# Optimization experiments

Measured on AMD Instinct MI355X. Metric: run time of the kernel, lower is better.

The kernel has to match this reference:

```python
import jax, jax.numpy as jnp
import numpy as np

B, T = 64, 20          # batch, caption length
C, HW = 512, 196       # cnn_channels, width*height (14x14)
V, E, U = 10000, 256, 512  # n_tokens, emb_size, lstm_units
MAX_NORM = 5.0


def setup_inputs() -> dict:
    key = jax.random.key(0)
    ks = jax.random.split(key, 12)
    s = 0.02
    return {
        "image_features": jax.random.normal(ks[0], (B, C, HW), jnp.float32),
        "captions_ix": jax.random.randint(ks[1], (B, T), 0, V, dtype=jnp.int32),
        "W_h0": jax.random.normal(ks[2], (U, C), jnp.float32) * s,
        "b_h0": jnp.zeros((U,), jnp.float32),
        "W_c0": jax.random.normal(ks[3], (U, C), jnp.float32) * s,
        "b_c0": jnp.zeros((U,), jnp.float32),
        "emb": jax.random.normal(ks[4], (V, E), jnp.float32) * s,
        "W_key": jax.random.normal(ks[5], (U, C), jnp.float32) * s,
        "b_key": jnp.zeros((U,), jnp.float32),
        "W_ih": jax.random.normal(ks[6], (4 * U, C + E), jnp.float32) * s,
        "b_ih": jnp.zeros((4 * U,), jnp.float32),
        "W_hh": jax.random.normal(ks[7], (4 * U, U), jnp.float32) * s,
        "b_hh": jnp.zeros((4 * U,), jnp.float32),
        "W_out": jax.random.normal(ks[8], (V, C + E + U), jnp.float32) * s,
        "b_out": jnp.zeros((V,), jnp.float32),
    }


def _caption_net(image_features, captions_ix, W_h0, b_h0, W_c0, b_c0, emb,
                 W_key, b_key, W_ih, b_ih, W_hh, b_hh, W_out, b_out):
    feats_mean = image_features.mean(axis=2)                # [B, C]
    hid0 = feats_mean @ W_h0.T + b_h0                       # [B, U]
    cell0 = feats_mean @ W_c0.T + b_c0                      # [B, U]
    feats = jnp.transpose(image_features, (0, 2, 1))        # [B, HW, C]
    keys = feats @ W_key.T + b_key                          # [B, HW, U]

    # nn.Embedding(max_norm=5): renorm rows whose L2 norm exceeds 5
    norms = jnp.linalg.norm(emb, axis=1, keepdims=True)
    emb_eff = emb * jnp.minimum(1.0, MAX_NORM / jnp.maximum(norms, 1e-12))
    cap_emb = emb_eff[captions_ix]                          # [B, T, E]

    inv_scale = 1.0 / (keys.shape[2] ** 0.5)

    def step(carry, emb_t):
        hid, cell = carry
        # scaled dot-product attention, query = current hidden state
        scores = jnp.einsum('bu,bku->bk', hid, keys) * inv_scale   # [B, HW]
        w = jax.nn.softmax(scores, axis=1)
        a = jnp.einsum('bk,bkc->bc', w, feats)                     # [B, C]
        x = jnp.concatenate([emb_t, a], axis=1)                    # [B, E+C]
        gates = x @ W_ih.T + b_ih + hid @ W_hh.T + b_hh            # [B, 4U]
        i, f, g, o = jnp.split(gates, 4, axis=1)
        cell = jax.nn.sigmoid(f) * cell + jax.nn.sigmoid(i) * jnp.tanh(g)
        hid = jax.nn.sigmoid(o) * jnp.tanh(cell)
        out = jnp.concatenate([hid, a, emb_t], axis=1)             # [B, U+C+E]
        return (hid, cell), (out, w)

    (_, _), (outs, attn) = jax.lax.scan(step, (hid0, cell0),
                                        jnp.transpose(cap_emb, (1, 0, 2)))
    outs = jnp.transpose(outs, (1, 0, 2))                   # [B, T, U+C+E]
    attn = jnp.transpose(attn, (1, 0, 2))                   # [B, T, HW]
    logits = outs @ W_out.T + b_out                         # [B, T, V]
    return logits, attn


def reference(image_features, captions_ix, W_h0, b_h0, W_c0, b_c0, emb,
              W_key, b_key, W_ih, b_ih, W_hh, b_hh, W_out, b_out):
    return _caption_net(image_features, captions_ix, W_h0, b_h0, W_c0, b_c0,
                        emb, W_key, b_key, W_ih, b_ih, W_hh, b_hh, W_out, b_out)
```

## Files before the change

### kernel.cpp

```cpp
#include <hip/hip_runtime.h>
#include <math.h>

#define B 64
#define T 20
#define C 512
#define HW 196
#define V 10000
#define E 256
#define U 512
#define G4U 2048
#define ODIM 1280
#define KTOT 1280
#define NBLK 64

typedef short bf8_t __attribute__((ext_vector_type(8)));
typedef float f4_t  __attribute__((ext_vector_type(4)));

__device__ __forceinline__ unsigned short f2bf(float f) {
    unsigned int u = __float_as_uint(f);
    return (unsigned short)((u + 0x7fffu + ((u >> 16) & 1u)) >> 16);
}
__device__ __forceinline__ float bf2f(unsigned short s) {
    return __uint_as_float((unsigned int)s << 16);
}
__device__ __forceinline__ float bflo(unsigned int kv) { return __uint_as_float(kv << 16); }
__device__ __forceinline__ float bfhi(unsigned int kv) { return __uint_as_float(kv & 0xffff0000u); }

__device__ __forceinline__ void coh_load4x2(const void* p0, const void* p1,
                                            uint4& r0, uint4& r1) {
    asm volatile("global_load_dwordx4 %0, %2, off sc0 sc1\n\t"
                 "global_load_dwordx4 %1, %3, off sc0 sc1\n\t"
                 "s_waitcnt vmcnt(0)"
                 : "=&v"(r0), "=&v"(r1) : "v"(p0), "v"(p1) : "memory");
}
__device__ __forceinline__ void coh_load4_issue(const void* p, uint4& r) {
    asm volatile("global_load_dwordx4 %0, %1, off sc0 sc1"
                 : "=&v"(r) : "v"(p) : "memory");
}
__device__ __forceinline__ void wait_vm0() {
    asm volatile("s_waitcnt vmcnt(0)" ::: "memory");
    __builtin_amdgcn_sched_barrier(0);
}
__device__ __forceinline__ void coh_store1f(void* p, float v) {
    asm volatile("global_store_dword %0, %1, off sc0 sc1" :: "v"(p), "v"(v) : "memory");
}
__device__ __forceinline__ void coh_store1u(void* p, unsigned int v) {
    asm volatile("global_store_dword %0, %1, off sc0 sc1" :: "v"(p), "v"(v) : "memory");
}
__device__ __forceinline__ void coh_store_us(void* p, unsigned int v) {
    asm volatile("global_store_short %0, %1, off sc0 sc1" :: "v"(p), "v"(v) : "memory");
}

__device__ __forceinline__ void gbar(int* bar) {
    asm volatile("s_waitcnt vmcnt(0)" ::: "memory");
    __syncthreads();
    if (threadIdx.x == 0) {
        int g = __hip_atomic_load(bar + 1, __ATOMIC_RELAXED, __HIP_MEMORY_SCOPE_AGENT);
        if (__hip_atomic_fetch_add(bar, 1, __ATOMIC_RELAXED, __HIP_MEMORY_SCOPE_AGENT) == NBLK - 1) {
            __hip_atomic_store(bar, 0, __ATOMIC_RELAXED, __HIP_MEMORY_SCOPE_AGENT);
            __hip_atomic_store(bar + 1, g + 1, __ATOMIC_RELEASE, __HIP_MEMORY_SCOPE_AGENT);
        } else {
            while (__hip_atomic_load(bar + 1, __ATOMIC_RELAXED, __HIP_MEMORY_SCOPE_AGENT) == g)
                __builtin_amdgcn_s_sleep(1);
        }
    }
    __syncthreads();
}

__global__ void k_mean(const float* __restrict__ img, float* __restrict__ fm,
                       int* __restrict__ bar) {
    if (blockIdx.x == 0 && threadIdx.x == 0) { bar[0] = 0; bar[1] = 0; }
    int wave = threadIdx.x >> 6;
    int lane = threadIdx.x & 63;
    int row = blockIdx.x * 4 + wave;
    const float* p = img + (size_t)row * HW;
    float s = p[lane] + p[lane + 64] + p[lane + 128];
    if (lane < 4) s += p[lane + 192];
    for (int off = 32; off > 0; off >>= 1) s += __shfl_down(s, off, 64);
    if (lane == 0) fm[row] = s * (1.0f / HW);
}

__global__ void k_init(const float* __restrict__ fm,
                       const float* __restrict__ W_h0, const float* __restrict__ b_h0,
                       const float* __restrict__ W_c0, const float* __restrict__ b_c0,
                       unsigned short* __restrict__ xb, float* __restrict__ cell) {
    int wv = blockIdx.x * 4 + (threadIdx.x >> 6);
    int lane = threadIdx.x & 63;
    int which = wv >> 15;
    int r = wv & 32767;
    int b = r >> 9, u = r & 511;
    const float* W = which ? W_c0 : W_h0;
    const float* bias = which ? b_c0 : b_h0;
    const float* f = fm + b * C;
    const float* w = W + (size_t)u * C;
    float s = 0.f;
    #pragma unroll
    for (int c = 0; c < C; c += 64) s += f[c + lane] * w[c + lane];
    for (int off = 32; off > 0; off >>= 1) s += __shfl_down(s, off, 64);
    if (lane == 0) {
        float v = s + bias[u];
        if (which) cell[r] = v;
        else       xb[(size_t)b * KTOT + 768 + u] = f2bf(v);
    }
}

__global__ void k_wkt(const float* __restrict__ Wk, float* __restrict__ WkT) {
    __shared__ float tile[64][65];
    int u0 = blockIdx.x * 64, c0 = blockIdx.y * 64;
    int x = threadIdx.x & 63, y0 = threadIdx.x >> 6;
    #pragma unroll
    for (int i = 0; i < 16; i++) {
        int r = y0 * 16 + i;
        tile[r][x] = Wk[(size_t)(u0 + r) * C + c0 + x];
    }
    __syncthreads();
    #pragma unroll
    for (int i = 0; i < 16; i++) {
        int r = y0 * 16 + i;
        WkT[(size_t)(c0 + r) * U + u0 + x] = tile[x][r];
    }
}

__global__ __launch_bounds__(256) void k_keys(const float* __restrict__ img,
        const float* __restrict__ WkT, const float* __restrict__ b_key,
        unsigned short* __restrict__ keys2) {
    __shared__ unsigned short st[32][200];
    int b = blockIdx.x >> 4;
    int u0 = (blockIdx.x & 15) * 32;
    int wave = __builtin_amdgcn_readfirstlane(threadIdx.x >> 6);
    int lane = threadIdx.x & 63;
    int lk = lane < 49 ? lane : 48;
    const f4_t* imgb = (const f4_t*)(img + (size_t)b * C * HW);
    f4_t acc[8];
    #pragma unroll
    for (int j = 0; j < 8; j++) acc[j] = (f4_t){0.f, 0.f, 0.f, 0.f};
    const float* wp = WkT + u0 + wave * 8;
    for (int c = 0; c < C; c++) {
        f4_t v = imgb[c * 49 + lk];
        const float* w = wp + (size_t)c * U;
        #pragma unroll
        for (int j = 0; j < 8; j++) acc[j] += v * w[j];
    }
    if (lane < 49) {
        #pragma unroll
        for (int j = 0; j < 8; j++) {
            float bk = b_key[u0 + wave * 8 + j];
            int ul = wave * 8 + j;
            int k = lane * 4;
            st[ul][k + 0] = f2bf(acc[j].x + bk);
            st[ul][k + 1] = f2bf(acc[j].y + bk);
            st[ul][k + 2] = f2bf(acc[j].z + bk);
            st[ul][k + 3] = f2bf(acc[j].w + bk);
        }
    }
    __syncthreads();
    int ui = threadIdx.x & 15;
    int kr = threadIdx.x >> 4;
    #pragma unroll
    for (int pass = 0; pass < 13; pass++) {
        int k = pass * 16 + kr;
        if (k < HW) {
            unsigned int lo = st[ui * 2][k];
            unsigned int hi = st[ui * 2 + 1][k];
            *(unsigned int*)&keys2[((size_t)b * HW + k) * U + u0 + ui * 2] = (hi << 16) | lo;
        }
    }
}

__global__ void k_wg(const float* __restrict__ W_ih, const float* __restrict__ W_hh,
                     unsigned short* __restrict__ Wg) {
    int j = blockIdx.x;
    int tid = threadIdx.x;
    const float* s1 = W_ih + (size_t)j * 768;
    const float* s2 = W_hh + (size_t)j * 512;
    unsigned short* dst = Wg + (size_t)j * KTOT;
    #pragma unroll
    for (int p = 0; p < 3; p++) dst[tid + p * 256] = f2bf(s1[tid + p * 256]);
    #pragma unroll
    for (int p = 0; p < 2; p++) dst[768 + tid + p * 256] = f2bf(s2[tid + p * 256]);
}

__global__ void k_emb(const int* __restrict__ ix, const float* __restrict__ emb,
                      unsigned short* __restrict__ outs) {
    int bt = blockIdx.x;
    int e = threadIdx.x;
    int row = ix[bt];
    float v = emb[(size_t)row * E + e];
    __shared__ float red[4];
    float sq = v * v;
    for (int off = 32; off > 0; off >>= 1) sq += __shfl_down(sq, off, 64);
    int wave = e >> 6, lane = e & 63;
    if (lane == 0) red[wave] = sq;
    __syncthreads();
    float norm = sqrtf(red[0] + red[1] + red[2] + red[3]);
    float scale = fminf(1.0f, 5.0f / fmaxf(norm, 1e-12f));
    outs[(size_t)bt * ODIM + (U + C) + e] = f2bf(v * scale);
}

__global__ __launch_bounds__(256) void k_wo(const float* __restrict__ W,
                                            unsigned short* __restrict__ Wb) {
    size_t i = ((size_t)blockIdx.x * 256 + threadIdx.x) * 8;
    float4 f0 = *(const float4*)(W + i);
    float4 f1 = *(const float4*)(W + i + 4);
    uint4 q;
    q.x = ((unsigned int)f2bf(f0.y) << 16) | f2bf(f0.x);
    q.y = ((unsigned int)f2bf(f0.w) << 16) | f2bf(f0.z);
    q.z = ((unsigned int)f2bf(f1.y) << 16) | f2bf(f1.x);
    q.w = ((unsigned int)f2bf(f1.w) << 16) | f2bf(f1.z);
    *(uint4*)(Wb + i) = q;
}

__global__ __launch_bounds__(256) void k_loop(
    unsigned short* __restrict__ outs, unsigned short* __restrict__ xb,
    const float* __restrict__ cell0, float* __restrict__ gates4,
    const unsigned short* __restrict__ keys2, const float* __restrict__ img,
    const float* __restrict__ b_ih, const float* __restrict__ b_hh,
    const unsigned short* __restrict__ Wg, float* __restrict__ attn,
    int* __restrict__ bar) {
    int b = blockIdx.x;
    int tid = threadIdx.x;
    int wave = __builtin_amdgcn_readfirstlane(tid >> 6);
    int lane = tid & 63;
    int m16 = lane & 15, quad = lane >> 4;
    __shared__ float hidS[U];
    __shared__ float wS[256];
    __shared__ float red[4];
    __shared__ unsigned short As2[64][72];
    __shared__ unsigned short Bs2[32][72];

    float c_r[2], bsum[2][4];
    #pragma unroll
    for (int p = 0; p < 2; p++) {
        int u = tid + p * 256;
        c_r[p] = cell0[(size_t)b * U + u];
        #pragma unroll
        for (int q = 0; q < 4; q++)
            bsum[p][q] = b_ih[q * 512 + u] + b_hh[q * 512 + u];
    }

    int j0g = blockIdx.x * 32;
    int r = tid >> 2, kq = tid & 3;
    int rb = tid >> 3, kb = tid & 7;
    int n16 = wave & 1, mpair = wave >> 1;

    for (int t = 0; t <= T; ++t) {
        if (t > 0) {
            const float* g0 = gates4 + (size_t)b * 2048 + tid * 4;
            uint4 r0, r1;
            coh_load4x2(g0, g0 + 1024, r0, r1);
            #pragma unroll
            for (int p = 0; p < 2; p++) {
                int u = tid + p * 256;
                float4 gv = p ? *(float4*)&r1 : *(float4*)&r0;
                float g0f = gv.x + bsum[p][0];
                float g1f = gv.y + bsum[p][1];
                float g2f = gv.z + bsum[p][2];
                float g3f = gv.w + bsum[p][3];
                float si = 1.f / (1.f + expf(-g0f));
                float sf = 1.f / (1.f + expf(-g1f));
                float tg = tanhf(g2f);
                float so = 1.f / (1.f + expf(-g3f));
                float cn = sf * c_r[p] + si * tg;
                c_r[p] = cn;
                float hn = so * tanhf(cn);
                hidS[u] = hn;
                unsigned int hv = f2bf(hn);
                outs[((size_t)b * T + (t - 1)) * ODIM + u] = (unsigned short)hv;
                coh_store_us(&xb[(size_t)b * KTOT + 768 + u], hv);
            }
        } else {
            #pragma unroll
            for (int p = 0; p < 2; p++) {
                int u = tid + p * 256;
                hidS[u] = bf2f(xb[(size_t)b * KTOT + 768 + u]);
            }
        }
        if (t == T) break;
        __syncthreads();

        float sc = 0.f;
        if (tid < HW) {
            const uint4* kr = (const uint4*)(keys2 + ((size_t)b * HW + tid) * U);
            float acc = 0.f;
            #pragma unroll 8
            for (int i = 0; i < 64; i++) {
                uint4 kv = kr[i];
                float4 h0 = *(const float4*)&hidS[i * 8];
                float4 h1 = *(const float4*)&hidS[i * 8 + 4];
                acc += bflo(kv.x) * h0.x + bfhi(kv.x) * h0.y
                     + bflo(kv.y) * h0.z + bfhi(kv.y) * h0.w
                     + bflo(kv.z) * h1.x + bfhi(kv.z) * h1.y
                     + bflo(kv.w) * h1.z + bfhi(kv.w) * h1.w;
            }
            sc = acc * 0.044194173824159216f;
        }
        {
            float v = (tid < HW) ? sc : -1e30f;
            float m = v;
            for (int off = 32; off > 0; off >>= 1) m = fmaxf(m, __shfl_down(m, off, 64));
            if (lane == 0) red[wave] = m;
            __syncthreads();
            m = fmaxf(fmaxf(red[0], red[1]), fmaxf(red[2], red[3]));
            float ex = (tid < HW) ? expf(v - m) : 0.f;
            float ssum = ex;
            for (int off = 32; off > 0; off >>= 1) ssum += __shfl_down(ssum, off, 64);
            __syncthreads();
            if (lane == 0) red[wave] = ssum;
            __syncthreads();
            ssum = red[0] + red[1] + red[2] + red[3];
            float w = ex / ssum;
            wS[tid] = w;
            if (tid < HW) attn[((size_t)b * T + t) * HW + tid] = w;
        }
        __syncthreads();

        {
            const float4* imgb = (const float4*)(img + (size_t)b * C * HW);
            #pragma unroll
            for (int p = 0; p < 2; p++) {
                int c = tid + p * 256;
                const float4* rr4 = imgb + c * 49;
                float acc = 0.f;
                for (int k4 = 0; k4 < 49; k4++) {
                    float4 vv = rr4[k4];
                    acc += wS[4 * k4] * vv.x + wS[4 * k4 + 1] * vv.y
                         + wS[4 * k4 + 2] * vv.z + wS[4 * k4 + 3] * vv.w;
                }
                unsigned int av = f2bf(acc);
                coh_store_us(&xb[(size_t)b * KTOT + 256 + c], av);
                outs[((size_t)b * T + t) * ODIM + U + c] = (unsigned short)av;
            }
        }
        if (tid < 128) {
            const unsigned int* src = (const unsigned int*)(outs + ((size_t)b * T + t) * ODIM);
            unsigned int* dst = (unsigned int*)(xb + (size_t)b * KTOT);
            coh_store1u(&dst[tid], src[512 + tid]);
        }

        gbar(bar);

        {
            f4_t acc2[2];
            acc2[0] = (f4_t){0.f, 0.f, 0.f, 0.f};
            acc2[1] = (f4_t){0.f, 0.f, 0.f, 0.f};
            const unsigned short* xrow = xb + (size_t)r * KTOT + kq * 16;
            const unsigned short* wrow = Wg + (size_t)(j0g + rb) * KTOT + kb * 8;
            uint4 a0, a1, bq;
            coh_load4x2(xrow, xrow + 8, a0, a1);
            bq = *(const uint4*)wrow;
            for (int k0 = 0; k0 < KTOT; k0 += 64) {
                *(uint4*)&As2[r][kq * 16]     = a0;
                *(uint4*)&As2[r][kq * 16 + 8] = a1;
                *(uint4*)&Bs2[rb][kb * 8]     = bq;
                __syncthreads();
                uint4 na0, na1, nbq;
                bool more = (k0 + 64 < KTOT);
                if (more) {
                    coh_load4_issue(xrow + k0 + 64, na0);
                    coh_load4_issue(xrow + k0 + 64 + 8, na1);
                    nbq = *(const uint4*)(wrow + k0 + 64);
                }
                #pragma unroll
                for (int h = 0; h < 2; h++) {
                    bf8_t bfr = *(const bf8_t*)&Bs2[n16 * 16 + m16][h * 32 + quad * 8];
                    #pragma unroll
                    for (int i2 = 0; i2 < 2; i2++) {
                        bf8_t afr = *(const bf8_t*)&As2[(mpair * 2 + i2) * 16 + m16][h * 32 + quad * 8];
                        acc2[i2] = __builtin_amdgcn_mfma_f32_16x16x32_bf16(afr, bfr, acc2[i2], 0, 0, 0);
                    }
                }
                if (more) {
                    wait_vm0();
                    a0 = na0; a1 = na1; bq = nbq;
                }
                __syncthreads();
            }
            int n = j0g + n16 * 16 + m16;
            int qq = n >> 9, uu = n & 511;
            float* gbase = gates4 + (size_t)uu * 4 + qq;
            #pragma unroll
            for (int i2 = 0; i2 < 2; i2++) {
                int mb = (mpair * 2 + i2) * 16 + quad * 4;
                #pragma unroll
                for (int rr = 0; rr < 4; rr++)
                    coh_store1f(gbase + (size_t)(mb + rr) * 2048, acc2[i2][rr]);
            }
        }

        gbar(bar);
    }
}

__global__ __launch_bounds__(256) void k_logits4(
    const unsigned short* __restrict__ A, const float* __restrict__ Wo,
    const float* __restrict__ bo, float* __restrict__ Cout) {
    __shared__ unsigned short As[128][72];
    __shared__ unsigned short Bs[128][72];
    int n0 = blockIdx.x * 128;
    int m0 = blockIdx.y * 128;
    int tid = threadIdx.x;
    int lane = tid & 63, wv = tid >> 6;
    int mw = (wv >> 1) * 64, nw = (wv & 1) * 64;
    int m16 = lane & 15, quad = lane >> 4;
    int srow = tid >> 1, shalf = tid & 1;

    f4_t acc[4][4];
    #pragma unroll
    for (int i = 0; i < 4; i++)
        #pragma unroll
        for (int j = 0; j < 4; j++)
            acc[i][j] = (f4_t){0.f, 0.f, 0.f, 0.f};

    for (int k0 = 0; k0 < KTOT; k0 += 64) {
        {
            const uint4* ap = (const uint4*)&A[(size_t)(m0 + srow) * KTOT + k0 + shalf * 32];
            uint4 a0 = ap[0], a1 = ap[1], a2 = ap[2], a3 = ap[3];
            uint4* dst = (uint4*)&As[srow][shalf * 32];
            dst[0] = a0; dst[1] = a1; dst[2] = a2; dst[3] = a3;
        }
        {
            int n = n0 + srow;
            uint4 q[4];
            if (n < V) {
                const float4* bp = (const float4*)&Wo[(size_t)n * KTOT + k0 + shalf * 32];
                #pragma unroll
                for (int g = 0; g < 4; g++) {
                    float4 f0 = bp[g * 2], f1 = bp[g * 2 + 1];
                    q[g].x = ((unsigned int)f2bf(f0.y) << 16) | f2bf(f0.x);
                    q[g].y = ((unsigned int)f2bf(f0.w) << 16) | f2bf(f0.z);
                    q[g].z = ((unsigned int)f2bf(f1.y) << 16) | f2bf(f1.x);
                    q[g].w = ((unsigned int)f2bf(f1.w) << 16) | f2bf(f1.z);
                }
            } else {
                #pragma unroll
                for (int g = 0; g < 4; g++) q[g] = (uint4){0u, 0u, 0u, 0u};
            }
            uint4* dst = (uint4*)&Bs[srow][shalf * 32];
            #pragma unroll
            for (int g = 0; g < 4; g++) dst[g] = q[g];
        }
        __syncthreads();
        #pragma unroll
        for (int h = 0; h < 2; h++) {
            bf8_t af[4], bf[4];
            #pragma unroll
            for (int i = 0; i < 4; i++)
                af[i] = *(const bf8_t*)&As[mw + i * 16 + m16][h * 32 + quad * 8];
            #pragma unroll
            for (int j = 0; j < 4; j++)
                bf[j] = *(const bf8_t*)&Bs[nw + j * 16 + m16][h * 32 + quad * 8];
            #pragma unroll
            for (int i = 0; i < 4; i++)
                #pragma unroll
                for (int j = 0; j < 4; j++)
                    acc[i][j] = __builtin_amdgcn_mfma_f32_16x16x32_bf16(af[i], bf[j], acc[i][j], 0, 0, 0);
        }
        __syncthreads();
    }

    #pragma unroll
    for (int j = 0; j < 4; j++) {
        int n = n0 + nw + j * 16 + m16;
        if (n >= V) continue;
        float bias = bo[n];
        #pragma unroll
        for (int i = 0; i < 4; i++) {
            int mb = m0 + mw + i * 16 + quad * 4;
            #pragma unroll
            for (int r = 0; r < 4; r++)
                Cout[(size_t)(mb + r) * V + n] = acc[i][j][r] + bias;
        }
    }
}

__global__ __launch_bounds__(256) void k_logits5(
    const unsigned short* __restrict__ A, const unsigned short* __restrict__ Wob,
    const float* __restrict__ bo, float* __restrict__ Cout) {
    __shared__ unsigned short As[128][72];
    __shared__ unsigned short Bs[128][72];
    int n0 = blockIdx.x * 128;
    int m0 = blockIdx.y * 128;
    int tid = threadIdx.x;
    int lane = tid & 63, wv = tid >> 6;
    int mw = (wv >> 1) * 64, nw = (wv & 1) * 64;
    int m16 = lane & 15, quad = lane >> 4;
    int srow = tid >> 1, shalf = tid & 1;

    f4_t acc[4][4];
    #pragma unroll
    for (int i = 0; i < 4; i++)
        #pragma unroll
        for (int j = 0; j < 4; j++)
            acc[i][j] = (f4_t){0.f, 0.f, 0.f, 0.f};

    for (int k0 = 0; k0 < KTOT; k0 += 64) {
        {
            const uint4* ap = (const uint4*)&A[(size_t)(m0 + srow) * KTOT + k0 + shalf * 32];
            uint4 a0 = ap[0], a1 = ap[1], a2 = ap[2], a3 = ap[3];
            uint4* dst = (uint4*)&As[srow][shalf * 32];
            dst[0] = a0; dst[1] = a1; dst[2] = a2; dst[3] = a3;
        }
        {
            int n = n0 + srow;
            uint4 q[4];
            if (n < V) {
                const uint4* bp = (const uint4*)&Wob[(size_t)n * KTOT + k0 + shalf * 32];
                #pragma unroll
                for (int g = 0; g < 4; g++) q[g] = bp[g];
            } else {
                #pragma unroll
                for (int g = 0; g < 4; g++) q[g] = (uint4){0u, 0u, 0u, 0u};
            }
            uint4* dst = (uint4*)&Bs[srow][shalf * 32];
            #pragma unroll
            for (int g = 0; g < 4; g++) dst[g] = q[g];
        }
        __syncthreads();
        #pragma unroll
        for (int h = 0; h < 2; h++) {
            bf8_t af[4], bf[4];
            #pragma unroll
            for (int i = 0; i < 4; i++)
                af[i] = *(const bf8_t*)&As[mw + i * 16 + m16][h * 32 + quad * 8];
            #pragma unroll
            for (int j = 0; j < 4; j++)
                bf[j] = *(const bf8_t*)&Bs[nw + j * 16 + m16][h * 32 + quad * 8];
            #pragma unroll
            for (int i = 0; i < 4; i++)
                #pragma unroll
                for (int j = 0; j < 4; j++)
                    acc[i][j] = __builtin_amdgcn_mfma_f32_16x16x32_bf16(af[i], bf[j], acc[i][j], 0, 0, 0);
        }
        __syncthreads();
    }

    #pragma unroll
    for (int j = 0; j < 4; j++) {
        int n = n0 + nw + j * 16 + m16;
        if (n >= V) continue;
        float bias = bo[n];
        #pragma unroll
        for (int i = 0; i < 4; i++) {
            int mb = m0 + mw + i * 16 + quad * 4;
            #pragma unroll
            for (int r = 0; r < 4; r++)
                Cout[(size_t)(mb + r) * V + n] = acc[i][j][r] + bias;
        }
    }
}

extern "C" void kernel_launch(void* const* d_in, const int* in_sizes, int n_in,
                              void* d_out, int out_size, void* d_ws, size_t ws_size,
                              hipStream_t stream) {
    const float* img   = (const float*)d_in[0];
    const int*   capix = (const int*)d_in[1];
    const float* W_h0  = (const float*)d_in[2];
    const float* b_h0  = (const float*)d_in[3];
    const float* W_c0  = (const float*)d_in[4];
    const float* b_c0  = (const float*)d_in[5];
    const float* emb   = (const float*)d_in[6];
    const float* W_key = (const float*)d_in[7];
    const float* b_key = (const float*)d_in[8];
    const float* W_ih  = (const float*)d_in[9];
    const float* b_ih  = (const float*)d_in[10];
    const float* W_hh  = (const float*)d_in[11];
    const float* b_hh  = (const float*)d_in[12];
    const float* W_out = (const float*)d_in[13];
    const float* b_out = (const float*)d_in[14];

    float* ws = (float*)d_ws;
    float* gates4    = ws;
    float* fm        = ws;
    float* cell      = gates4 + 131072;
    float* WkT       = cell + 32768;
    unsigned short* Wg    = (unsigned short*)(WkT + 262144);
    unsigned short* xb    = Wg + 2621440;
    unsigned short* outs  = xb + 81920;
    unsigned short* keys2 = outs + (size_t)B * T * ODIM;
    int* bar = (int*)(keys2 + (size_t)B * HW * U);
    const size_t WOB_OFF = 23232576;
    unsigned short* Wob = (unsigned short*)((char*)d_ws + WOB_OFF);
    bool use_wob = ws_size >= WOB_OFF + (size_t)V * KTOT * 2;

    float* logits = (float*)d_out;
    float* attn   = logits + (size_t)B * T * V;

    k_mean<<<(B * C) / 4, 256, 0, stream>>>(img, fm, bar);
    k_init<<<(2 * B * U) / 4, 256, 0, stream>>>(fm, W_h0, b_h0, W_c0, b_c0, xb, cell);
    k_wkt<<<dim3(8, 8), 256, 0, stream>>>(W_key, WkT);
    k_keys<<<B * 16, 256, 0, stream>>>(img, WkT, b_key, keys2);
    k_wg<<<G4U, 256, 0, stream>>>(W_ih, W_hh, Wg);
    k_emb<<<B * T, 256, 0, stream>>>(capix, emb, outs);
    if (use_wob)
        k_wo<<<(V * KTOT) / 2048, 256, 0, stream>>>(W_out, Wob);

    k_loop<<<NBLK, 256, 0, stream>>>(outs, xb, cell, gates4, keys2, img,
                                     b_ih, b_hh, Wg, attn, bar);

    if (use_wob)
        k_logits5<<<dim3((V + 127) / 128, (B * T) / 128), 256, 0, stream>>>(outs, Wob, b_out, logits);
    else
        k_logits4<<<dim3((V + 127) / 128, (B * T) / 128), 256, 0, stream>>>(outs, W_out, b_out, logits);
}
```

Measured before the change: 1.230 ms.

## Replace atomic grid barrier with flag-based barrier and restage recurrent gate GEMM

Replaces the atomic counter grid barrier with a flag-array barrier: each block writes its epoch to its own padded slot, block 0 polls all slots with one wave and then publishes a release flag. The recurrent gate GEMM now stages the full xb activations into swizzled LDS in four 320-wide K chunks and reads the Wg weight fragments straight from global memory, replacing the double-buffered 64-wide K loop. The barrier flags reuse the WkT workspace region and are zeroed in k_emb. This aims to cut barrier latency and the syncthreads count per timestep, at the cost of uncached global weight reads inside the MFMA loop and a two-hop barrier path through block 0.

```diff
diff --git a/kernel.cpp b/kernel.cpp
--- a/kernel.cpp
+++ b/kernel.cpp
@@ -50,26 +50,37 @@
 __device__ __forceinline__ void coh_store_us(void* p, unsigned int v) {
     asm volatile("global_store_short %0, %1, off sc0 sc1" :: "v"(p), "v"(v) : "memory");
 }
-
-__device__ __forceinline__ void gbar(int* bar) {
+__device__ __forceinline__ int coh_load_int(const int* p) {
+    int v;
+    asm volatile("global_load_dword %0, %1, off sc0 sc1\n\t"
+                 "s_waitcnt vmcnt(0)"
+                 : "=v"(v) : "v"(p) : "memory");
+    return v;
+}
+__device__ __forceinline__ void coh_store_int(int* p, int v) {
+    asm volatile("global_store_dword %0, %1, off sc0 sc1" :: "v"(p), "v"(v) : "memory");
+}
+
+__device__ __forceinline__ void gbarf(int* barf, int e) {
     asm volatile("s_waitcnt vmcnt(0)" ::: "memory");
     __syncthreads();
-    if (threadIdx.x == 0) {
-        int g = __hip_atomic_load(bar + 1, __ATOMIC_RELAXED, __HIP_MEMORY_SCOPE_AGENT);
-        if (__hip_atomic_fetch_add(bar, 1, __ATOMIC_RELAXED, __HIP_MEMORY_SCOPE_AGENT) == NBLK - 1) {
-            __hip_atomic_store(bar, 0, __ATOMIC_RELAXED, __HIP_MEMORY_SCOPE_AGENT);
-            __hip_atomic_store(bar + 1, g + 1, __ATOMIC_RELEASE, __HIP_MEMORY_SCOPE_AGENT);
-        } else {
-            while (__hip_atomic_load(bar + 1, __ATOMIC_RELAXED, __HIP_MEMORY_SCOPE_AGENT) == g)
-                __builtin_amdgcn_s_sleep(1);
+    int tid = threadIdx.x;
+    if (blockIdx.x == 0) {
+        if (tid == 0) coh_store_int(barf + 16, e);
+        if (tid < 64) {
+            while (!__all(coh_load_int(barf + 16 + tid * 16) >= e)) {}
+            if (tid == 0) coh_store_int(barf, e);
+        }
+    } else {
+        if (tid == 0) {
+            coh_store_int(barf + 16 + blockIdx.x * 16, e);
+            while (coh_load_int(barf) < e) {}
         }
     }
     __syncthreads();
 }
 
-__global__ void k_mean(const float* __restrict__ img, float* __restrict__ fm,
-                       int* __restrict__ bar) {
-    if (blockIdx.x == 0 && threadIdx.x == 0) { bar[0] = 0; bar[1] = 0; }
+__global__ void k_mean(const float* __restrict__ img, float* __restrict__ fm) {
     int wave = threadIdx.x >> 6;
     int lane = threadIdx.x & 63;
     int row = blockIdx.x * 4 + wave;
@@ -181,9 +192,12 @@
 }
 
 __global__ void k_emb(const int* __restrict__ ix, const float* __restrict__ emb,
-                      unsigned short* __restrict__ outs) {
+                      unsigned short* __restrict__ outs, int* __restrict__ barf) {
     int bt = blockIdx.x;
     int e = threadIdx.x;
+    if (bt == 0) {
+        for (int i = e; i < 1040; i += 256) barf[i] = 0;
+    }
     int row = ix[bt];
     float v = emb[(size_t)row * E + e];
     __shared__ float red[4];
@@ -216,7 +230,7 @@
     const unsigned short* __restrict__ keys2, const float* __restrict__ img,
     const float* __restrict__ b_ih, const float* __restrict__ b_hh,
     const unsigned short* __restrict__ Wg, float* __restrict__ attn,
-    int* __restrict__ bar) {
+    int* __restrict__ barf) {
     int b = blockIdx.x;
     int tid = threadIdx.x;
     int wave = __builtin_amdgcn_readfirstlane(tid >> 6);
@@ -225,8 +239,7 @@
     __shared__ float hidS[U];
     __shared__ float wS[256];
     __shared__ float red[4];
-    __shared__ unsigned short As2[64][72];
-    __shared__ unsigned short Bs2[32][72];
+    __shared__ unsigned short As[64 * 320];
 
     float c_r[2], bsum[2][4];
     #pragma unroll
@@ -239,9 +252,9 @@
     }
 
     int j0g = blockIdx.x * 32;
-    int r = tid >> 2, kq = tid & 3;
-    int rb = tid >> 3, kb = tid & 7;
-    int n16 = wave & 1, mpair = wave >> 1;
+    int srow = tid >> 2, scol = tid & 3;
+    int arow = wave * 16 + m16;
+    int ep = 0;
 
     for (int t = 0; t <= T; ++t) {
         if (t > 0) {
@@ -337,57 +350,51 @@
             coh_store1u(&dst[tid], src[512 + tid]);
         }
 
-        gbar(bar);
+        ++ep; gbarf(barf, ep);
 
         {
             f4_t acc2[2];
             acc2[0] = (f4_t){0.f, 0.f, 0.f, 0.f};
             acc2[1] = (f4_t){0.f, 0.f, 0.f, 0.f};
-            const unsigned short* xrow = xb + (size_t)r * KTOT + kq * 16;
-            const unsigned short* wrow = Wg + (size_t)(j0g + rb) * KTOT + kb * 8;
-            uint4 a0, a1, bq;
-            coh_load4x2(xrow, xrow + 8, a0, a1);
-            bq = *(const uint4*)wrow;
-            for (int k0 = 0; k0 < KTOT; k0 += 64) {
-                *(uint4*)&As2[r][kq * 16]     = a0;
-                *(uint4*)&As2[r][kq * 16 + 8] = a1;
-                *(uint4*)&Bs2[rb][kb * 8]     = bq;
-                __syncthreads();
-                uint4 na0, na1, nbq;
-                bool more = (k0 + 64 < KTOT);
-                if (more) {
-                    coh_load4_issue(xrow + k0 + 64, na0);
-                    coh_load4_issue(xrow + k0 + 64 + 8, na1);
-                    nbq = *(const uint4*)(wrow + k0 + 64);
-                }
-                #pragma unroll
-                for (int h = 0; h < 2; h++) {
-                    bf8_t bfr = *(const bf8_t*)&Bs2[n16 * 16 + m16][h * 32 + quad * 8];
-                    #pragma unroll
-                    for (int i2 = 0; i2 < 2; i2++) {
-                        bf8_t afr = *(const bf8_t*)&As2[(mpair * 2 + i2) * 16 + m16][h * 32 + quad * 8];
-                        acc2[i2] = __builtin_amdgcn_mfma_f32_16x16x32_bf16(afr, bfr, acc2[i2], 0, 0, 0);
-                    }
-                }
-                if (more) {
-                    wait_vm0();
-                    a0 = na0; a1 = na1; bq = nbq;
+            #pragma unroll 1
+            for (int s = 0; s < 4; s++) {
+                int kbase = s * 320;
+                uint4 ra[10];
+                #pragma unroll
+                for (int p = 0; p < 10; p++)
+                    coh_load4_issue(&xb[(size_t)srow * KTOT + kbase + (scol + 4 * p) * 8], ra[p]);
+                wait_vm0();
+                #pragma unroll
+                for (int p = 0; p < 10; p++) {
+                    int chunk = scol + 4 * p;
+                    *(uint4*)&As[srow * 320 + ((chunk * 8) ^ ((srow & 7) << 3))] = ra[p];
                 }
                 __syncthreads();
-            }
-            int n = j0g + n16 * 16 + m16;
-            int qq = n >> 9, uu = n & 511;
-            float* gbase = gates4 + (size_t)uu * 4 + qq;
-            #pragma unroll
-            for (int i2 = 0; i2 < 2; i2++) {
-                int mb = (mpair * 2 + i2) * 16 + quad * 4;
-                #pragma unroll
-                for (int rr = 0; rr < 4; rr++)
-                    coh_store1f(gbase + (size_t)(mb + rr) * 2048, acc2[i2][rr]);
-            }
-        }
-
-        gbar(bar);
+                #pragma unroll
+                for (int c = 0; c < 10; c++) {
+                    int kl = c * 32 + quad * 8;
+                    bf8_t afr = *(const bf8_t*)&As[arow * 320 + (kl ^ ((m16 & 7) << 3))];
+                    int kg = kbase + kl;
+                    bf8_t b0 = *(const bf8_t*)&Wg[(size_t)(j0g + m16) * KTOT + kg];
+                    bf8_t b1 = *(const bf8_t*)&Wg[(size_t)(j0g + 16 + m16) * KTOT + kg];
+                    acc2[0] = __builtin_amdgcn_mfma_f32_16x16x32_bf16(afr, b0, acc2[0], 0, 0, 0);
+                    acc2[1] = __builtin_amdgcn_mfma_f32_16x16x32_bf16(afr, b1, acc2[1], 0, 0, 0);
+                }
+                __syncthreads();
+            }
+            #pragma unroll
+            for (int nt = 0; nt < 2; nt++) {
+                int n = j0g + nt * 16 + m16;
+                int qq = n >> 9, uu = n & 511;
+                #pragma unroll
+                for (int rr = 0; rr < 4; rr++) {
+                    int bb = wave * 16 + quad * 4 + rr;
+                    coh_store1f(&gates4[((size_t)bb * 512 + uu) * 4 + qq], acc2[nt][rr]);
+                }
+            }
+        }
+
+        ++ep; gbarf(barf, ep);
     }
 }
 
@@ -573,11 +580,11 @@
     float* fm        = ws;
     float* cell      = gates4 + 131072;
     float* WkT       = cell + 32768;
+    int*   barf      = (int*)WkT;
     unsigned short* Wg    = (unsigned short*)(WkT + 262144);
     unsigned short* xb    = Wg + 2621440;
     unsigned short* outs  = xb + 81920;
     unsigned short* keys2 = outs + (size_t)B * T * ODIM;
-    int* bar = (int*)(keys2 + (size_t)B * HW * U);
     const size_t WOB_OFF = 23232576;
     unsigned short* Wob = (unsigned short*)((char*)d_ws + WOB_OFF);
     bool use_wob = ws_size >= WOB_OFF + (size_t)V * KTOT * 2;
@@ -585,17 +592,17 @@
     float* logits = (float*)d_out;
     float* attn   = logits + (size_t)B * T * V;
 
-    k_mean<<<(B * C) / 4, 256, 0, stream>>>(img, fm, bar);
+    k_mean<<<(B * C) / 4, 256, 0, stream>>>(img, fm);
     k_init<<<(2 * B * U) / 4, 256, 0, stream>>>(fm, W_h0, b_h0, W_c0, b_c0, xb, cell);
     k_wkt<<<dim3(8, 8), 256, 0, stream>>>(W_key, WkT);
     k_keys<<<B * 16, 256, 0, stream>>>(img, WkT, b_key, keys2);
     k_wg<<<G4U, 256, 0, stream>>>(W_ih, W_hh, Wg);
-    k_emb<<<B * T, 256, 0, stream>>>(capix, emb, outs);
+    k_emb<<<B * T, 256, 0, stream>>>(capix, emb, outs, barf);
     if (use_wob)
         k_wo<<<(V * KTOT) / 2048, 256, 0, stream>>>(W_out, Wob);
 
     k_loop<<<NBLK, 256, 0, stream>>>(outs, xb, cell, gates4, keys2, img,
-                                     b_ih, b_hh, Wg, attn, bar);
+                                     b_ih, b_hh, Wg, attn, barf);
 
     if (use_wob)
         k_logits5<<<dim3((V + 127) / 128, (B * T) / 128), 256, 0, stream>>>(outs, Wob, b_out, logits);
```

After: 1.243 ms. Within noise of the previous version (+1.0%).
